# Performance work log

Hardware: AMD Instinct MI355X
Metric: run time of the kernel (lower is better)

## Reference

```python
import jax, jax.numpy as jnp
import numpy as np

INF = jnp.float32(np.inf)
LAMBDA_VAL = 1.0
NUM_CLASSES = 10

def setup_inputs() -> dict:
    key = jax.random.key(0)
    k1, k2, k3 = jax.random.split(key, 3)
    N, P, D = 65536, 2048, 64
    x = jax.random.normal(k1, (N, D), dtype=jnp.float32)
    y = jax.random.randint(k2, (N,), 0, NUM_CLASSES)
    prototypes = jax.random.normal(k3, (P, D), dtype=jnp.float32)
    prototype_labels = jnp.arange(P) % NUM_CLASSES
    return {"x": x, "y": y, "prototypes": prototypes, "prototype_labels": prototype_labels}

def _cdist(x, p):
    # Euclidean pairwise distances via the gemm expansion (matches torch.cdist default
    x2 = jnp.sum(x * x, axis=1, keepdims=True)          # [N, 1]
    p2 = jnp.sum(p * p, axis=1)                          # [P]
    sq = x2 + p2[None, :] - 2.0 * (x @ p.T)              # [N, P]
    return jnp.sqrt(jnp.maximum(sq, 0.0))

def reference(x, y, prototypes, prototype_labels):
    distances = _cdist(x, prototypes)                    # [N, P]
    same = prototype_labels[None, :] == y[:, None]       # [N, P] bool
    pos = jnp.min(jnp.where(same, distances, INF), axis=1)   # [N]
    neg = jnp.min(jnp.where(~same, distances, INF), axis=1)  # [N]
    mu = (pos - neg) / (pos + neg)
    loss = jnp.mean(jax.nn.sigmoid(LAMBDA_VAL * mu))
    return loss
```

## Files before the change

kernel.cpp:

```cpp
#include <hip/hip_runtime.h>
#include <math.h>

#define NROWS  65536
#define NPROTO 2048
#define DDIM   64
#define NCLS   10

#define CLS_SLOTS   208
#define CLS_FFRAGS  13
#define CLS_STRIDE  27648
#define CLS_P2_OFF  26624

#define WS_IMG_BYTES   (NCLS * CLS_STRIDE)
#define WS_XA_OFF      WS_IMG_BYTES
#define WS_XA_BYTES    (1024 * 8192)
#define WS_MINS_OFF    (WS_XA_OFF + WS_XA_BYTES)
#define WS_MINS_BYTES  (NCLS * NROWS * 2)
#define WS_X2_OFF      (WS_MINS_OFF + WS_MINS_BYTES)

typedef __attribute__((ext_vector_type(8))) short bf16x8;
typedef __attribute__((ext_vector_type(4))) float f32x4;
typedef __attribute__((ext_vector_type(4))) unsigned int u32x4;

__device__ inline unsigned int f2bf(float f) {
    unsigned int u = __float_as_uint(f);
    return (u + 0x7FFFu + ((u >> 16) & 1u)) >> 16;
}

template <int CTRL>
__device__ inline float rorMin(float v) {
    int t = __builtin_amdgcn_update_dpp(0, __float_as_int(v), CTRL, 0xF, 0xF, false);
    return fminf(v, __int_as_float(t));
}

__global__ __launch_bounds__(256) void prep_kernel(
        const float* __restrict__ x, const float* __restrict__ protos,
        char* __restrict__ wsB, float* __restrict__ out) {
    if (blockIdx.x < 65) {
        int t = blockIdx.x * 256 + threadIdx.x;
        int s = t >> 3, jj = t & 7;
        int L = s / CLS_SLOTS;
        int j = s - L * CLS_SLOTS;
        int cnt = (L < 8) ? 205 : 204;
        bool real = (j < cnt);
        float v[8] = {0.f, 0.f, 0.f, 0.f, 0.f, 0.f, 0.f, 0.f};
        if (real) {
            const float* src = protos + (L + 10 * j) * DDIM + jj * 8;
            float4 a = *(const float4*)src;
            float4 b = *(const float4*)(src + 4);
            v[0] = a.x; v[1] = a.y; v[2] = a.z; v[3] = a.w;
            v[4] = b.x; v[5] = b.y; v[6] = b.z; v[7] = b.w;
        }
        float ss = 0.f;
#pragma unroll
        for (int i = 0; i < 8; i++) ss = fmaf(v[i], v[i], ss);
        ss += __shfl_xor(ss, 1, 64);
        ss += __shfl_xor(ss, 2, 64);
        ss += __shfl_xor(ss, 4, 64);
        unsigned int w[4];
#pragma unroll
        for (int i = 0; i < 4; i++) {
            unsigned int lo = f2bf(-2.f * v[2 * i]);
            unsigned int hi = f2bf(-2.f * v[2 * i + 1]);
            w[i] = lo | (hi << 16);
        }
        size_t base = (size_t)L * CLS_STRIDE;
        *(u32x4*)(wsB + base + (size_t)(j * 8 + (jj ^ (j & 7))) * 16) =
            (u32x4){w[0], w[1], w[2], w[3]};
        if (jj == 0)
            *(float*)(wsB + base + CLS_P2_OFF + j * 4) =
                real ? ss : __builtin_inff();
        if (t == 0) out[0] = 0.f;
    } else {
        int t = (blockIdx.x - 65) * 256 + threadIdx.x;
        int row = t >> 3, j = t & 7;
        const float* src = x + (size_t)row * DDIM + j * 8;
        float4 a = *(const float4*)src;
        float4 b = *(const float4*)(src + 4);
        float v[8] = {a.x, a.y, a.z, a.w, b.x, b.y, b.z, b.w};
        float ss = 0.f;
#pragma unroll
        for (int i = 0; i < 8; i++) ss = fmaf(v[i], v[i], ss);
        ss += __shfl_xor(ss, 1, 64);
        ss += __shfl_xor(ss, 2, 64);
        ss += __shfl_xor(ss, 4, 64);
        unsigned int w[4];
#pragma unroll
        for (int i = 0; i < 4; i++) {
            unsigned int lo = f2bf(v[2 * i]);
            unsigned int hi = f2bf(v[2 * i + 1]);
            w[i] = lo | (hi << 16);
        }
        int rt = row >> 6, m = (row & 63) >> 4, l15 = row & 15;
        int k = j >> 2, q = j & 3;
        size_t off = (size_t)rt * 8192 + m * 2048 + k * 1024 + (q * 16 + l15) * 16;
        *(u32x4*)(wsB + WS_XA_OFF + off) = (u32x4){w[0], w[1], w[2], w[3]};
        if (j == 0) *(float*)(wsB + WS_X2_OFF + (size_t)row * 4) = ss;
    }
}

__global__ __launch_bounds__(512) void glvq_main(
        const char* __restrict__ wsB, _Float16* __restrict__ wsMins) {
    __shared__ __align__(16) char ldsImg[CLS_STRIDE];

    const int tid  = threadIdx.x;
    const int wave = tid >> 6;
    const int lane = tid & 63;
    const int quad = lane >> 4;
    const int l15  = lane & 15;
    const int label = blockIdx.y;
    const float CINF = __builtin_inff();

    const int rowTile = blockIdx.x * 8 + wave;
    const char* xATile = wsB + WS_XA_OFF + (size_t)rowTile * 8192;
    bf16x8 afrag[4][2];
#pragma unroll
    for (int m = 0; m < 4; m++)
#pragma unroll
        for (int k = 0; k < 2; k++)
            afrag[m][k] = *(const bf16x8*)(xATile + m * 2048 + k * 1024 + lane * 16);

    {
        const char* src = wsB + (size_t)label * CLS_STRIDE;
#pragma unroll
        for (int it = 0; it < 3; it++) {
            int ub = it * 512 + wave * 64;
            __builtin_amdgcn_global_load_lds(
                (const __attribute__((address_space(1))) void*)(src + (size_t)ub * 16 + lane * 16),
                (__attribute__((address_space(3))) void*)(ldsImg + (size_t)ub * 16),
                16, 0, 0);
        }
        if (wave < 2) {
            int ub = 1536 + wave * 64;
            __builtin_amdgcn_global_load_lds(
                (const __attribute__((address_space(1))) void*)(src + (size_t)ub * 16 + lane * 16),
                (__attribute__((address_space(3))) void*)(ldsImg + (size_t)ub * 16),
                16, 0, 0);
        }
        if (wave == 2) {
            int ub = 1664;
            __builtin_amdgcn_global_load_lds(
                (const __attribute__((address_space(1))) void*)(src + (size_t)ub * 16 + lane * 16),
                (__attribute__((address_space(3))) void*)(ldsImg + (size_t)ub * 16),
                16, 0, 0);
        }
    }
    asm volatile("s_waitcnt vmcnt(0)" ::: "memory");
    __syncthreads();

    float mMin[4][4];
#pragma unroll
    for (int m = 0; m < 4; m++)
#pragma unroll
        for (int r = 0; r < 4; r++) mMin[m][r] = CINF;

#pragma unroll
    for (int f = 0; f < CLS_FFRAGS; f++) {
        const int s = f * 16 + l15;
        float p2v = *(const float*)(ldsImg + CLS_P2_OFF + s * 4);
        f32x4 p2f = (f32x4){p2v, p2v, p2v, p2v};
        bf16x8 b0 = *(const bf16x8*)(ldsImg + (size_t)(s * 8 + (quad ^ (l15 & 7))) * 16);
        bf16x8 b1 = *(const bf16x8*)(ldsImg + (size_t)(s * 8 + ((4 + quad) ^ (l15 & 7))) * 16);
        f32x4 acc[4];
#pragma unroll
        for (int m = 0; m < 4; m++)
            acc[m] = __builtin_amdgcn_mfma_f32_16x16x32_bf16(
                afrag[m][0], b0, p2f, 0, 0, 0);
#pragma unroll
        for (int m = 0; m < 4; m++)
            acc[m] = __builtin_amdgcn_mfma_f32_16x16x32_bf16(
                afrag[m][1], b1, acc[m], 0, 0, 0);
#pragma unroll
        for (int m = 0; m < 4; m++)
#pragma unroll
            for (int r = 0; r < 4; r++)
                mMin[m][r] = fminf(mMin[m][r], acc[m][r]);
    }

#pragma unroll
    for (int m = 0; m < 4; m++)
#pragma unroll
        for (int r = 0; r < 4; r++) {
            float v = mMin[m][r];
            v = rorMin<0x128>(v);
            v = rorMin<0x124>(v);
            v = rorMin<0x122>(v);
            v = rorMin<0x121>(v);
            mMin[m][r] = v;
        }

    if (l15 == 0) {
        _Float16* plane = wsMins + (size_t)label * NROWS + rowTile * 64;
#pragma unroll
        for (int m = 0; m < 4; m++)
#pragma unroll
            for (int r = 0; r < 4; r++)
                plane[m * 16 + quad * 4 + r] = (_Float16)mMin[m][r];
    }
}

__global__ __launch_bounds__(256) void combine_kernel(
        const int* __restrict__ y, const _Float16* __restrict__ wsMins,
        const float* __restrict__ wsX2, float* __restrict__ out) {
    int row = blockIdx.x * 256 + threadIdx.x;
    int yr = y[row];
    float pos = 0.f, neg = __builtin_inff();
#pragma unroll
    for (int L = 0; L < NCLS; L++) {
        float d = (float)wsMins[(size_t)L * NROWS + row];
        bool isPos = (L == yr);
        pos = isPos ? d : pos;
        neg = isPos ? neg : fminf(neg, d);
    }
    float x2v = wsX2[row];
    float sp = sqrtf(fmaxf(x2v + pos, 0.f));
    float sn = sqrtf(fmaxf(x2v + neg, 0.f));
    float mu = (sp - sn) / (sp + sn);
    float s = 1.f / (1.f + __expf(-mu));

    __shared__ float red[256];
    red[threadIdx.x] = s;
    __syncthreads();
#pragma unroll
    for (int off = 128; off > 0; off >>= 1) {
        if (threadIdx.x < off) red[threadIdx.x] += red[threadIdx.x + off];
        __syncthreads();
    }
    if (threadIdx.x == 0) atomicAdd(out, red[0] * (1.f / (float)NROWS));
}

extern "C" void kernel_launch(void* const* d_in, const int* in_sizes, int n_in,
                              void* d_out, int out_size, void* d_ws, size_t ws_size,
                              hipStream_t stream) {
    const float* x      = (const float*)d_in[0];
    const int*   y      = (const int*)d_in[1];
    const float* protos = (const float*)d_in[2];
    float* out = (float*)d_out;

    char*      wsB    = (char*)d_ws;
    _Float16*  wsMins = (_Float16*)((char*)d_ws + WS_MINS_OFF);
    float*     wsX2   = (float*)((char*)d_ws + WS_X2_OFF);

    prep_kernel<<<65 + NROWS * 8 / 256, 256, 0, stream>>>(x, protos, wsB, out);
    glvq_main<<<dim3(128, 10), 512, 0, stream>>>(wsB, wsMins);
    combine_kernel<<<NROWS / 256, 256, 0, stream>>>(y, wsMins, wsX2, out);
}
```

Measured before the change: 91.51 us.

## Fuse x conversion, per-class min, and loss reduction into one kernel

Replaces the three-kernel pipeline (prep of x and prototypes, per-class MFMA min, combine) with a prototype-only prep plus a single fused kernel. Each block now converts its 128 rows of x to bf16 fragments in registers, loops over all ten class images with double-buffered LDS loads, keeps pos/neg minima in registers and reduces the sigmoid loss directly. This removes the bf16 x staging buffer, the fp16 per-class minima plane and the extra kernel launch. In exchange each wave handles 32 rows instead of 64, and there is a block-wide barrier per class, which cuts MFMA reuse per B fragment and adds serialization.

After: 101.3 us. +10.7%, slower.

```diff
diff --git a/kernel.cpp b/kernel.cpp
--- a/kernel.cpp
+++ b/kernel.cpp
@@ -2,7 +2,6 @@
 #include <math.h>
 
 #define NROWS  65536
-#define NPROTO 2048
 #define DDIM   64
 #define NCLS   10
 
@@ -11,13 +10,6 @@
 #define CLS_STRIDE  27648
 #define CLS_P2_OFF  26624
 
-#define WS_IMG_BYTES   (NCLS * CLS_STRIDE)
-#define WS_XA_OFF      WS_IMG_BYTES
-#define WS_XA_BYTES    (1024 * 8192)
-#define WS_MINS_OFF    (WS_XA_OFF + WS_XA_BYTES)
-#define WS_MINS_BYTES  (NCLS * NROWS * 2)
-#define WS_X2_OFF      (WS_MINS_OFF + WS_MINS_BYTES)
-
 typedef __attribute__((ext_vector_type(8))) short bf16x8;
 typedef __attribute__((ext_vector_type(4))) float f32x4;
 typedef __attribute__((ext_vector_type(4))) unsigned int u32x4;
@@ -34,214 +26,230 @@
 }
 
 __global__ __launch_bounds__(256) void prep_kernel(
-        const float* __restrict__ x, const float* __restrict__ protos,
-        char* __restrict__ wsB, float* __restrict__ out) {
-    if (blockIdx.x < 65) {
-        int t = blockIdx.x * 256 + threadIdx.x;
-        int s = t >> 3, jj = t & 7;
-        int L = s / CLS_SLOTS;
-        int j = s - L * CLS_SLOTS;
-        int cnt = (L < 8) ? 205 : 204;
-        bool real = (j < cnt);
-        float v[8] = {0.f, 0.f, 0.f, 0.f, 0.f, 0.f, 0.f, 0.f};
-        if (real) {
-            const float* src = protos + (L + 10 * j) * DDIM + jj * 8;
-            float4 a = *(const float4*)src;
-            float4 b = *(const float4*)(src + 4);
-            v[0] = a.x; v[1] = a.y; v[2] = a.z; v[3] = a.w;
-            v[4] = b.x; v[5] = b.y; v[6] = b.z; v[7] = b.w;
-        }
-        float ss = 0.f;
-#pragma unroll
-        for (int i = 0; i < 8; i++) ss = fmaf(v[i], v[i], ss);
-        ss += __shfl_xor(ss, 1, 64);
-        ss += __shfl_xor(ss, 2, 64);
-        ss += __shfl_xor(ss, 4, 64);
-        unsigned int w[4];
-#pragma unroll
-        for (int i = 0; i < 4; i++) {
-            unsigned int lo = f2bf(-2.f * v[2 * i]);
-            unsigned int hi = f2bf(-2.f * v[2 * i + 1]);
-            w[i] = lo | (hi << 16);
-        }
-        size_t base = (size_t)L * CLS_STRIDE;
-        *(u32x4*)(wsB + base + (size_t)(j * 8 + (jj ^ (j & 7))) * 16) =
-            (u32x4){w[0], w[1], w[2], w[3]};
-        if (jj == 0)
-            *(float*)(wsB + base + CLS_P2_OFF + j * 4) =
-                real ? ss : __builtin_inff();
-        if (t == 0) out[0] = 0.f;
-    } else {
-        int t = (blockIdx.x - 65) * 256 + threadIdx.x;
-        int row = t >> 3, j = t & 7;
-        const float* src = x + (size_t)row * DDIM + j * 8;
+        const float* __restrict__ protos, char* __restrict__ wsB,
+        float* __restrict__ out) {
+    int t = blockIdx.x * 256 + threadIdx.x;
+    int s = t >> 3, jj = t & 7;
+    int L = s / CLS_SLOTS;
+    int j = s - L * CLS_SLOTS;
+    int cnt = (L < 8) ? 205 : 204;
+    bool real = (j < cnt);
+    float v[8] = {0.f, 0.f, 0.f, 0.f, 0.f, 0.f, 0.f, 0.f};
+    if (real) {
+        const float* src = protos + (L + 10 * j) * DDIM + jj * 8;
         float4 a = *(const float4*)src;
         float4 b = *(const float4*)(src + 4);
-        float v[8] = {a.x, a.y, a.z, a.w, b.x, b.y, b.z, b.w};
-        float ss = 0.f;
-#pragma unroll
-        for (int i = 0; i < 8; i++) ss = fmaf(v[i], v[i], ss);
-        ss += __shfl_xor(ss, 1, 64);
-        ss += __shfl_xor(ss, 2, 64);
-        ss += __shfl_xor(ss, 4, 64);
-        unsigned int w[4];
-#pragma unroll
-        for (int i = 0; i < 4; i++) {
-            unsigned int lo = f2bf(v[2 * i]);
-            unsigned int hi = f2bf(v[2 * i + 1]);
-            w[i] = lo | (hi << 16);
-        }
-        int rt = row >> 6, m = (row & 63) >> 4, l15 = row & 15;
-        int k = j >> 2, q = j & 3;
-        size_t off = (size_t)rt * 8192 + m * 2048 + k * 1024 + (q * 16 + l15) * 16;
-        *(u32x4*)(wsB + WS_XA_OFF + off) = (u32x4){w[0], w[1], w[2], w[3]};
-        if (j == 0) *(float*)(wsB + WS_X2_OFF + (size_t)row * 4) = ss;
-    }
-}
-
-__global__ __launch_bounds__(512) void glvq_main(
-        const char* __restrict__ wsB, _Float16* __restrict__ wsMins) {
-    __shared__ __align__(16) char ldsImg[CLS_STRIDE];
+        v[0] = a.x; v[1] = a.y; v[2] = a.z; v[3] = a.w;
+        v[4] = b.x; v[5] = b.y; v[6] = b.z; v[7] = b.w;
+    }
+    float ss = 0.f;
+#pragma unroll
+    for (int i = 0; i < 8; i++) ss = fmaf(v[i], v[i], ss);
+    ss += __shfl_xor(ss, 1, 64);
+    ss += __shfl_xor(ss, 2, 64);
+    ss += __shfl_xor(ss, 4, 64);
+    unsigned int w[4];
+#pragma unroll
+    for (int i = 0; i < 4; i++) {
+        unsigned int lo = f2bf(-2.f * v[2 * i]);
+        unsigned int hi = f2bf(-2.f * v[2 * i + 1]);
+        w[i] = lo | (hi << 16);
+    }
+    size_t base = (size_t)L * CLS_STRIDE;
+    *(u32x4*)(wsB + base + (size_t)(j * 8 + (jj ^ (j & 7))) * 16) =
+        (u32x4){w[0], w[1], w[2], w[3]};
+    if (jj == 0)
+        *(float*)(wsB + base + CLS_P2_OFF + j * 4) =
+            real ? ss : __builtin_inff();
+    if (t == 0) out[0] = 0.f;
+}
+
+__global__ __launch_bounds__(256) void glvq_fused(
+        const float* __restrict__ x, const int* __restrict__ y,
+        const char* __restrict__ wsB, float* __restrict__ out) {
+    __shared__ __align__(16) char ldsImg[2][CLS_STRIDE];
+    __shared__ float ldsX2[4 * 32];
+    __shared__ float ldsRed[4];
 
     const int tid  = threadIdx.x;
     const int wave = tid >> 6;
     const int lane = tid & 63;
     const int quad = lane >> 4;
     const int l15  = lane & 15;
-    const int label = blockIdx.y;
     const float CINF = __builtin_inff();
-
-    const int rowTile = blockIdx.x * 8 + wave;
-    const char* xATile = wsB + WS_XA_OFF + (size_t)rowTile * 8192;
-    bf16x8 afrag[4][2];
-#pragma unroll
-    for (int m = 0; m < 4; m++)
-#pragma unroll
-        for (int k = 0; k < 2; k++)
-            afrag[m][k] = *(const bf16x8*)(xATile + m * 2048 + k * 1024 + lane * 16);
+    const int rowBase = blockIdx.x * 128 + wave * 32;
+    int c0 = blockIdx.x % NCLS;
 
     {
-        const char* src = wsB + (size_t)label * CLS_STRIDE;
-#pragma unroll
-        for (int it = 0; it < 3; it++) {
-            int ub = it * 512 + wave * 64;
-            __builtin_amdgcn_global_load_lds(
-                (const __attribute__((address_space(1))) void*)(src + (size_t)ub * 16 + lane * 16),
-                (__attribute__((address_space(3))) void*)(ldsImg + (size_t)ub * 16),
-                16, 0, 0);
-        }
-        if (wave < 2) {
-            int ub = 1536 + wave * 64;
-            __builtin_amdgcn_global_load_lds(
-                (const __attribute__((address_space(1))) void*)(src + (size_t)ub * 16 + lane * 16),
-                (__attribute__((address_space(3))) void*)(ldsImg + (size_t)ub * 16),
-                16, 0, 0);
-        }
-        if (wave == 2) {
-            int ub = 1664;
-            __builtin_amdgcn_global_load_lds(
-                (const __attribute__((address_space(1))) void*)(src + (size_t)ub * 16 + lane * 16),
-                (__attribute__((address_space(3))) void*)(ldsImg + (size_t)ub * 16),
-                16, 0, 0);
-        }
-    }
+        const char* src = wsB + (size_t)c0 * CLS_STRIDE;
+#pragma unroll
+        for (int it = 0; it < 7; it++) {
+            int i = wave + it * 4;
+            if (i < 27) {
+                int ub = i * 64;
+                __builtin_amdgcn_global_load_lds(
+                    (const __attribute__((address_space(1))) void*)(src + (size_t)(ub + lane) * 16),
+                    (__attribute__((address_space(3))) void*)(&ldsImg[0][0] + (size_t)ub * 16),
+                    16, 0, 0);
+            }
+        }
+    }
+
+    bf16x8 afrag[2][2];
+#pragma unroll
+    for (int m = 0; m < 2; m++) {
+        float ss = 0.f;
+#pragma unroll
+        for (int k = 0; k < 2; k++) {
+            const float* src = x + (size_t)(rowBase + m * 16 + l15) * DDIM + k * 32 + quad * 8;
+            float4 a = *(const float4*)src;
+            float4 b = *(const float4*)(src + 4);
+            float v[8] = {a.x, a.y, a.z, a.w, b.x, b.y, b.z, b.w};
+            unsigned int w[4];
+#pragma unroll
+            for (int i = 0; i < 4; i++) {
+                ss = fmaf(v[2 * i],     v[2 * i],     ss);
+                ss = fmaf(v[2 * i + 1], v[2 * i + 1], ss);
+                w[i] = f2bf(v[2 * i]) | (f2bf(v[2 * i + 1]) << 16);
+            }
+            union { u32x4 u; bf16x8 h; } cvt;
+            cvt.u = (u32x4){w[0], w[1], w[2], w[3]};
+            afrag[m][k] = cvt.h;
+        }
+        ss += __shfl_xor(ss, 16, 64);
+        ss += __shfl_xor(ss, 32, 64);
+        if (quad == 0) ldsX2[wave * 32 + m * 16 + l15] = ss;
+    }
+
+    int yv[2][4];
+#pragma unroll
+    for (int m = 0; m < 2; m++)
+#pragma unroll
+        for (int r = 0; r < 4; r++)
+            yv[m][r] = y[rowBase + m * 16 + quad * 4 + r];
+
+    float pos[2][4], neg[2][4];
+#pragma unroll
+    for (int m = 0; m < 2; m++)
+#pragma unroll
+        for (int r = 0; r < 4; r++) { pos[m][r] = 0.f; neg[m][r] = CINF; }
+
     asm volatile("s_waitcnt vmcnt(0)" ::: "memory");
     __syncthreads();
 
-    float mMin[4][4];
-#pragma unroll
-    for (int m = 0; m < 4; m++)
-#pragma unroll
-        for (int r = 0; r < 4; r++) mMin[m][r] = CINF;
-
-#pragma unroll
-    for (int f = 0; f < CLS_FFRAGS; f++) {
-        const int s = f * 16 + l15;
-        float p2v = *(const float*)(ldsImg + CLS_P2_OFF + s * 4);
-        f32x4 p2f = (f32x4){p2v, p2v, p2v, p2v};
-        bf16x8 b0 = *(const bf16x8*)(ldsImg + (size_t)(s * 8 + (quad ^ (l15 & 7))) * 16);
-        bf16x8 b1 = *(const bf16x8*)(ldsImg + (size_t)(s * 8 + ((4 + quad) ^ (l15 & 7))) * 16);
-        f32x4 acc[4];
-#pragma unroll
-        for (int m = 0; m < 4; m++)
-            acc[m] = __builtin_amdgcn_mfma_f32_16x16x32_bf16(
-                afrag[m][0], b0, p2f, 0, 0, 0);
-#pragma unroll
-        for (int m = 0; m < 4; m++)
-            acc[m] = __builtin_amdgcn_mfma_f32_16x16x32_bf16(
-                afrag[m][1], b1, acc[m], 0, 0, 0);
-#pragma unroll
-        for (int m = 0; m < 4; m++)
-#pragma unroll
-            for (int r = 0; r < 4; r++)
-                mMin[m][r] = fminf(mMin[m][r], acc[m][r]);
-    }
-
-#pragma unroll
-    for (int m = 0; m < 4; m++)
-#pragma unroll
-        for (int r = 0; r < 4; r++) {
-            float v = mMin[m][r];
-            v = rorMin<0x128>(v);
-            v = rorMin<0x124>(v);
-            v = rorMin<0x122>(v);
-            v = rorMin<0x121>(v);
-            mMin[m][r] = v;
-        }
-
+    float x2r[2][4];
+#pragma unroll
+    for (int m = 0; m < 2; m++)
+#pragma unroll
+        for (int r = 0; r < 4; r++)
+            x2r[m][r] = ldsX2[wave * 32 + m * 16 + quad * 4 + r];
+
+    for (int ci = 0; ci < NCLS; ci++) {
+        const char* buf = &ldsImg[ci & 1][0];
+
+        if (ci < NCLS - 1) {
+            int cn = c0 + ci + 1; if (cn >= NCLS) cn -= NCLS;
+            const char* src = wsB + (size_t)cn * CLS_STRIDE;
+            char* dst = &ldsImg[(ci + 1) & 1][0];
+#pragma unroll
+            for (int it = 0; it < 7; it++) {
+                int i = wave + it * 4;
+                if (i < 27) {
+                    int ub = i * 64;
+                    __builtin_amdgcn_global_load_lds(
+                        (const __attribute__((address_space(1))) void*)(src + (size_t)(ub + lane) * 16),
+                        (__attribute__((address_space(3))) void*)(dst + (size_t)ub * 16),
+                        16, 0, 0);
+                }
+            }
+        }
+
+        float mMin[2][4];
+#pragma unroll
+        for (int m = 0; m < 2; m++)
+#pragma unroll
+            for (int r = 0; r < 4; r++) mMin[m][r] = CINF;
+
+#pragma unroll
+        for (int f = 0; f < CLS_FFRAGS; f++) {
+            const int s = f * 16 + l15;
+            float p2v = *(const float*)(buf + CLS_P2_OFF + s * 4);
+            f32x4 p2f = (f32x4){p2v, p2v, p2v, p2v};
+            bf16x8 b0 = *(const bf16x8*)(buf + (size_t)(s * 8 + (quad ^ (l15 & 7))) * 16);
+            bf16x8 b1 = *(const bf16x8*)(buf + (size_t)(s * 8 + ((4 + quad) ^ (l15 & 7))) * 16);
+            f32x4 acc[2];
+#pragma unroll
+            for (int m = 0; m < 2; m++)
+                acc[m] = __builtin_amdgcn_mfma_f32_16x16x32_bf16(
+                    afrag[m][0], b0, p2f, 0, 0, 0);
+#pragma unroll
+            for (int m = 0; m < 2; m++)
+                acc[m] = __builtin_amdgcn_mfma_f32_16x16x32_bf16(
+                    afrag[m][1], b1, acc[m], 0, 0, 0);
+#pragma unroll
+            for (int m = 0; m < 2; m++)
+#pragma unroll
+                for (int r = 0; r < 4; r++)
+                    mMin[m][r] = fminf(mMin[m][r], acc[m][r]);
+        }
+
+#pragma unroll
+        for (int m = 0; m < 2; m++)
+#pragma unroll
+            for (int r = 0; r < 4; r++) {
+                float vmin = mMin[m][r];
+                vmin = rorMin<0x128>(vmin);
+                vmin = rorMin<0x124>(vmin);
+                vmin = rorMin<0x122>(vmin);
+                vmin = rorMin<0x121>(vmin);
+                mMin[m][r] = vmin;
+            }
+
+        int cc = c0 + ci; if (cc >= NCLS) cc -= NCLS;
+#pragma unroll
+        for (int m = 0; m < 2; m++)
+#pragma unroll
+            for (int r = 0; r < 4; r++) {
+                float d = mMin[m][r];
+                bool isPos = (cc == yv[m][r]);
+                pos[m][r] = isPos ? d : pos[m][r];
+                neg[m][r] = isPos ? neg[m][r] : fminf(neg[m][r], d);
+            }
+
+        asm volatile("s_waitcnt vmcnt(0)" ::: "memory");
+        __syncthreads();
+    }
+
+    float sum = 0.f;
     if (l15 == 0) {
-        _Float16* plane = wsMins + (size_t)label * NROWS + rowTile * 64;
-#pragma unroll
-        for (int m = 0; m < 4; m++)
-#pragma unroll
-            for (int r = 0; r < 4; r++)
-                plane[m * 16 + quad * 4 + r] = (_Float16)mMin[m][r];
-    }
-}
-
-__global__ __launch_bounds__(256) void combine_kernel(
-        const int* __restrict__ y, const _Float16* __restrict__ wsMins,
-        const float* __restrict__ wsX2, float* __restrict__ out) {
-    int row = blockIdx.x * 256 + threadIdx.x;
-    int yr = y[row];
-    float pos = 0.f, neg = __builtin_inff();
-#pragma unroll
-    for (int L = 0; L < NCLS; L++) {
-        float d = (float)wsMins[(size_t)L * NROWS + row];
-        bool isPos = (L == yr);
-        pos = isPos ? d : pos;
-        neg = isPos ? neg : fminf(neg, d);
-    }
-    float x2v = wsX2[row];
-    float sp = sqrtf(fmaxf(x2v + pos, 0.f));
-    float sn = sqrtf(fmaxf(x2v + neg, 0.f));
-    float mu = (sp - sn) / (sp + sn);
-    float s = 1.f / (1.f + __expf(-mu));
-
-    __shared__ float red[256];
-    red[threadIdx.x] = s;
+#pragma unroll
+        for (int m = 0; m < 2; m++)
+#pragma unroll
+            for (int r = 0; r < 4; r++) {
+                float sp = sqrtf(fmaxf(x2r[m][r] + pos[m][r], 0.f));
+                float sn = sqrtf(fmaxf(x2r[m][r] + neg[m][r], 0.f));
+                float mu = (sp - sn) / (sp + sn);
+                sum += 1.f / (1.f + __expf(-mu));
+            }
+    }
+    sum += __shfl_xor(sum, 16, 64);
+    sum += __shfl_xor(sum, 32, 64);
+    if (lane == 0) ldsRed[wave] = sum;
     __syncthreads();
-#pragma unroll
-    for (int off = 128; off > 0; off >>= 1) {
-        if (threadIdx.x < off) red[threadIdx.x] += red[threadIdx.x + off];
-        __syncthreads();
-    }
-    if (threadIdx.x == 0) atomicAdd(out, red[0] * (1.f / (float)NROWS));
+    if (tid == 0)
+        atomicAdd(out, (ldsRed[0] + ldsRed[1] + ldsRed[2] + ldsRed[3]) *
+                           (1.f / (float)NROWS));
 }
 
 extern "C" void kernel_launch(void* const* d_in, const int* in_sizes, int n_in,
                               void* d_out, int out_size, void* d_ws, size_t ws_size,
                               hipStream_t stream) {
     const float* x      = (const float*)d_in[0];
-    const int*   y      = (const int*)d_in[1];
+    const int*   yp     = (const int*)d_in[1];
     const float* protos = (const float*)d_in[2];
     float* out = (float*)d_out;
-
-    char*      wsB    = (char*)d_ws;
-    _Float16*  wsMins = (_Float16*)((char*)d_ws + WS_MINS_OFF);
-    float*     wsX2   = (float*)((char*)d_ws + WS_X2_OFF);
-
-    prep_kernel<<<65 + NROWS * 8 / 256, 256, 0, stream>>>(x, protos, wsB, out);
-    glvq_main<<<dim3(128, 10), 512, 0, stream>>>(wsB, wsMins);
-    combine_kernel<<<NROWS / 256, 256, 0, stream>>>(y, wsMins, wsX2, out);
-}
+    char*  wsB = (char*)d_ws;
+
+    prep_kernel<<<65, 256, 0, stream>>>(protos, wsB, out);
+    glvq_fused<<<512, 256, 0, stream>>>(x, yp, wsB, out);
+}
```
